# Kernel optimization log

Hardware: AMD Instinct MI355X
Metric: run time of the kernel (lower is better)

## Reference

```python
import jax, jax.numpy as jnp
import numpy as np

D_MODEL = 1024
NHEAD = 16
HEAD_DIM = D_MODEL // NHEAD


def setup_inputs() -> dict:
    key = jax.random.key(0)
    k1, k2, k3 = jax.random.split(key, 3)
    x = jax.random.normal(k1, (4, 2048, D_MODEL), dtype=jnp.float32)
    # xavier_uniform init for weights, zero bias
    lim_qkv = float(np.sqrt(6.0 / (D_MODEL + 3 * D_MODEL)))
    w_qkv = jax.random.uniform(k2, (3 * D_MODEL, D_MODEL), jnp.float32, -lim_qkv, lim_qkv)
    b_qkv = jnp.zeros((3 * D_MODEL,), jnp.float32)
    lim_o = float(np.sqrt(6.0 / (D_MODEL + D_MODEL)))
    w_o = jax.random.uniform(k3, (D_MODEL, D_MODEL), jnp.float32, -lim_o, lim_o)
    b_o = jnp.zeros((D_MODEL,), jnp.float32)
    return {"x": x, "w_qkv": w_qkv, "b_qkv": b_qkv, "w_o": w_o, "b_o": b_o}


def reference(x, w_qkv, b_qkv, w_o, b_o):
    B, S, _ = x.shape
    qkv = x @ w_qkv.T + b_qkv                      # [B,S,3D]
    qkv = qkv.reshape(B, S, NHEAD, 3 * HEAD_DIM).transpose(0, 2, 1, 3)  # [B,H,S,3d]
    q, k, v = jnp.split(qkv, 3, axis=-1)           # each [B,H,S,d]
    scale = 1.0 / jnp.sqrt(jnp.asarray(HEAD_DIM, x.dtype))
    logits = jnp.einsum('bhqd,bhkd->bhqk', q, k) * scale
    attn = jax.nn.softmax(logits, axis=-1)
    vals = jnp.einsum('bhqk,bhkd->bhqd', attn, v)  # [B,H,S,d]
    vals = vals.transpose(0, 2, 1, 3).reshape(B, S, D_MODEL)
    return vals @ w_o.T + b_o
```

## Files before the change

kernel.cpp:

```cpp
#include <hip/hip_runtime.h>
#include <hip/hip_bf16.h>
#include <stdint.h>

typedef unsigned short u16;
typedef __bf16 bf16x8 __attribute__((ext_vector_type(8)));
typedef short s16x4 __attribute__((ext_vector_type(4)));
typedef float f32x4 __attribute__((ext_vector_type(4)));
typedef u16 u16x4v __attribute__((ext_vector_type(4)));

#define AS1 __attribute__((address_space(1)))
#define AS3 __attribute__((address_space(3)))

__device__ __forceinline__ void gld_lds16(const u16* g, u16* l) {
    __builtin_amdgcn_global_load_lds((const AS1 uint32_t*)g, (AS3 uint32_t*)l, 16, 0, 0);
}

__device__ __forceinline__ u16 f2bf(float f) {
    union { float f; uint32_t u; } v; v.f = f;
    uint32_t u = v.u;
    return (u16)((u + 0x7FFFu + ((u >> 16) & 1u)) >> 16);
}

#define QSCALE 0.18033688011112042f

__global__ void cast_f32_bf16(const float* __restrict__ in, u16* __restrict__ out, int n4) {
    int i = blockIdx.x * blockDim.x + threadIdx.x;
    if (i < n4) {
        float4 f = ((const float4*)in)[i];
        u16x4v o;
        o.x = f2bf(f.x); o.y = f2bf(f.y); o.z = f2bf(f.z); o.w = f2bf(f.w);
        ((u16x4v*)out)[i] = o;
    }
}

template <int MODE>
__global__ __launch_bounds__(256, 2) void gemm_bt(
    const u16* __restrict__ A, const u16* __restrict__ B,
    const float* __restrict__ bias, float* __restrict__ Cf,
    u16* __restrict__ qb, u16* __restrict__ kb, u16* __restrict__ vT,
    int K, int ldc)
{
    __shared__ __align__(16) u16 As[128 * 32];
    __shared__ __align__(16) u16 Bs[128 * 32];
    const int tid = threadIdx.x;
    const int lane = tid & 63;
    const int w = tid >> 6;
    const int wm = (w >> 1) << 6;
    const int wn = (w & 1) << 6;
    const int r = lane & 15;
    const int q = lane >> 4;
    const int m0 = blockIdx.y << 7;
    const int n0 = blockIdx.x << 7;

    const f32x4 zero4 = {0.f, 0.f, 0.f, 0.f};
    f32x4 acc[4][4];
#pragma unroll
    for (int i = 0; i < 4; ++i)
#pragma unroll
        for (int j = 0; j < 4; ++j) acc[i][j] = zero4;

    const int nk = K >> 5;
    for (int kt = 0; kt < nk; ++kt) {
        const int kk = kt << 5;
#pragma unroll
        for (int p = 0; p < 2; ++p) {
            const int idx = (p << 8) + tid;
            const int row = idx >> 2;
            const int cg = ((idx & 3) - (row >> 1)) & 3;
            gld_lds16(A + (m0 + row) * K + kk + (cg << 3), &As[idx << 3]);
            gld_lds16(B + (n0 + row) * K + kk + (cg << 3), &Bs[idx << 3]);
        }
        __syncthreads();
        bf16x8 af[4], bf[4];
#pragma unroll
        for (int i = 0; i < 4; ++i) {
            const int ra = wm + (i << 4) + r;
            af[i] = *(const bf16x8*)&As[((ra << 2) + ((q + (ra >> 1)) & 3)) << 3];
            const int rb = wn + (i << 4) + r;
            bf[i] = *(const bf16x8*)&Bs[((rb << 2) + ((q + (rb >> 1)) & 3)) << 3];
        }
#pragma unroll
        for (int i = 0; i < 4; ++i)
#pragma unroll
            for (int j = 0; j < 4; ++j)
                acc[i][j] = __builtin_amdgcn_mfma_f32_16x16x32_bf16(af[i], bf[j], acc[i][j], 0, 0, 0);
        __syncthreads();
    }

#pragma unroll
    for (int j = 0; j < 4; ++j) {
        const int col = n0 + wn + (j << 4) + r;
        const float bv = bias[col];
        if (MODE == 0) {
#pragma unroll
            for (int i = 0; i < 4; ++i)
#pragma unroll
                for (int ii = 0; ii < 4; ++ii) {
                    const int rowg = m0 + wm + (i << 4) + (q << 2) + ii;
                    Cf[rowg * ldc + col] = acc[i][j][ii] + bv;
                }
        } else {
            const int c0 = n0 + wn + (j << 4);
            const int h = c0 / 192;
            const int rem = c0 - h * 192;
            const int region = rem >> 6;
            const int colp = (h << 6) + (rem - (region << 6)) + r;
            if (region == 0) {
#pragma unroll
                for (int i = 0; i < 4; ++i)
#pragma unroll
                    for (int ii = 0; ii < 4; ++ii) {
                        const int rowg = m0 + wm + (i << 4) + (q << 2) + ii;
                        qb[rowg * 1024 + colp] = f2bf((acc[i][j][ii] + bv) * QSCALE);
                    }
            } else if (region == 1) {
#pragma unroll
                for (int i = 0; i < 4; ++i)
#pragma unroll
                    for (int ii = 0; ii < 4; ++ii) {
                        const int rowg = m0 + wm + (i << 4) + (q << 2) + ii;
                        kb[rowg * 1024 + colp] = f2bf(acc[i][j][ii] + bv);
                    }
            } else {
#pragma unroll
                for (int i = 0; i < 4; ++i) {
                    const int rowg0 = m0 + wm + (i << 4) + (q << 2);
                    u16x4v vv;
                    vv.x = f2bf(acc[i][j][0] + bv);
                    vv.y = f2bf(acc[i][j][1] + bv);
                    vv.z = f2bf(acc[i][j][2] + bv);
                    vv.w = f2bf(acc[i][j][3] + bv);
                    *(u16x4v*)&vT[(size_t)colp * 8192 + rowg0] = vv;
                }
            }
        }
    }
}

__global__ __launch_bounds__(256, 4) void attn(
    const u16* __restrict__ qb, const u16* __restrict__ kb,
    const u16* __restrict__ vT, u16* __restrict__ vals)
{
    __shared__ __align__(16) u16 Qs[128 * 64];
    __shared__ __align__(16) u16 Ks[64 * 64];
    __shared__ __align__(16) u16 VTs[64 * 64];

    const int tid = threadIdx.x;
    const int lane = tid & 63;
    const int w = tid >> 6;
    const int r = lane & 15;
    const int q = lane >> 4;
    const int h = blockIdx.x;
    const int q0 = blockIdx.y << 7;
    const int b = blockIdx.z;
    const size_t rowbase = (size_t)b * 2048;

#pragma unroll
    for (int p = 0; p < 4; ++p) {
        const int idx = (p << 8) + tid;
        const int row = idx >> 3;
        const int cg = ((idx & 7) - row) & 7;
        gld_lds16(qb + (rowbase + q0 + row) * 1024 + (h << 6) + (cg << 3), &Qs[idx << 3]);
    }

    const f32x4 zero4 = {0.f, 0.f, 0.f, 0.f};
    f32x4 oacc[4][2];
    float lpart[2];
#pragma unroll
    for (int ht = 0; ht < 4; ++ht)
#pragma unroll
        for (int nt = 0; nt < 2; ++nt) oacc[ht][nt] = zero4;
    lpart[0] = 0.f; lpart[1] = 0.f;

    for (int kt = 0; kt < 32; ++kt) {
        const int k0 = kt << 6;
#pragma unroll
        for (int p = 0; p < 2; ++p) {
            const int idx = (p << 8) + tid;
            const int row = idx >> 3;
            const int cg = ((idx & 7) - row) & 7;
            gld_lds16(kb + (rowbase + k0 + row) * 1024 + (h << 6) + (cg << 3), &Ks[idx << 3]);
        }
#pragma unroll
        for (int p = 0; p < 2; ++p) {
            const int idx = (p << 8) + tid;
            const int hd = idx >> 3;
            const int pc = idx & 7;
            const int lc = (pc - hd - (hd >> 3)) & 7;
            gld_lds16(vT + (size_t)((h << 6) + hd) * 8192 + rowbase + k0 + (lc << 3), &VTs[idx << 3]);
        }
        __syncthreads();

        f32x4 sacc[4][2];
#pragma unroll
        for (int mt = 0; mt < 4; ++mt)
#pragma unroll
            for (int nt = 0; nt < 2; ++nt) sacc[mt][nt] = zero4;
#pragma unroll
        for (int ks = 0; ks < 2; ++ks) {
            const int L = (ks << 2) + q;
            bf16x8 bq[2], ak[4];
#pragma unroll
            for (int nt = 0; nt < 2; ++nt) {
                const int row = (w << 5) + (nt << 4) + r;
                bq[nt] = *(const bf16x8*)&Qs[(row << 6) + (((L + row) & 7) << 3)];
            }
#pragma unroll
            for (int mt = 0; mt < 4; ++mt) {
                const int row = (mt << 4) + r;
                ak[mt] = *(const bf16x8*)&Ks[(row << 6) + (((L + row) & 7) << 3)];
            }
#pragma unroll
            for (int mt = 0; mt < 4; ++mt)
#pragma unroll
                for (int nt = 0; nt < 2; ++nt)
                    sacc[mt][nt] = __builtin_amdgcn_mfma_f32_16x16x32_bf16(ak[mt], bq[nt], sacc[mt][nt], 0, 0, 0);
        }

        s16x4 pb[4][2];
#pragma unroll
        for (int mt = 0; mt < 4; ++mt) {
#pragma unroll
            for (int nt = 0; nt < 2; ++nt) {
                const float e0 = __builtin_amdgcn_exp2f(sacc[mt][nt][0]);
                const float e1 = __builtin_amdgcn_exp2f(sacc[mt][nt][1]);
                const float e2 = __builtin_amdgcn_exp2f(sacc[mt][nt][2]);
                const float e3 = __builtin_amdgcn_exp2f(sacc[mt][nt][3]);
                lpart[nt] += (e0 + e1) + (e2 + e3);
                union { __hip_bfloat162 h2[2]; s16x4 v; } u;
                u.h2[0] = __float22bfloat162_rn(float2{e0, e1});
                u.h2[1] = __float22bfloat162_rn(float2{e2, e3});
                pb[mt][nt] = u.v;
            }
        }

#pragma unroll
        for (int mt = 0; mt < 4; ++mt) {
            s16x4 av[4];
#pragma unroll
            for (int ht = 0; ht < 4; ++ht) {
                const int hd = (ht << 4) + r;
                const int chunk = (mt << 1) + (q >> 1);
                const int pc = (chunk + hd + (hd >> 3)) & 7;
                av[ht] = *(const s16x4*)&VTs[(hd << 6) + (pc << 3) + ((q & 1) << 2)];
            }
#pragma unroll
            for (int ht = 0; ht < 4; ++ht)
#pragma unroll
                for (int nt = 0; nt < 2; ++nt)
                    oacc[ht][nt] = __builtin_amdgcn_mfma_f32_16x16x16bf16_1k(av[ht], pb[mt][nt], oacc[ht][nt], 0, 0, 0);
        }
        __syncthreads();
    }

#pragma unroll
    for (int nt = 0; nt < 2; ++nt) {
        float l = lpart[nt];
        l += __shfl_xor(l, 16, 64);
        l += __shfl_xor(l, 32, 64);
        const float inv = 1.f / l;
        const int srow = q0 + (w << 5) + (nt << 4) + r;
#pragma unroll
        for (int ht = 0; ht < 4; ++ht) {
            u16x4v vv;
            vv.x = f2bf(oacc[ht][nt][0] * inv);
            vv.y = f2bf(oacc[ht][nt][1] * inv);
            vv.z = f2bf(oacc[ht][nt][2] * inv);
            vv.w = f2bf(oacc[ht][nt][3] * inv);
            const int col = (h << 6) + (ht << 4) + (q << 2);
            *(u16x4v*)&vals[(rowbase + srow) * 1024 + col] = vv;
        }
    }
}

extern "C" void kernel_launch(void* const* d_in, const int* in_sizes, int n_in,
                              void* d_out, int out_size, void* d_ws, size_t ws_size,
                              hipStream_t stream) {
    (void)in_sizes; (void)n_in; (void)out_size; (void)ws_size;
    const float* x     = (const float*)d_in[0];
    const float* w_qkv = (const float*)d_in[1];
    const float* b_qkv = (const float*)d_in[2];
    const float* w_o   = (const float*)d_in[3];
    const float* b_o   = (const float*)d_in[4];
    float* out = (float*)d_out;

    char* ws = (char*)d_ws;
    u16* xb    = (u16*)(ws);
    u16* wqkvb = (u16*)(ws + (size_t)(16 << 20));
    u16* wob   = (u16*)(ws + (size_t)(22 << 20));
    u16* qb    = (u16*)(ws + (size_t)(24 << 20));
    u16* kb    = (u16*)(ws + (size_t)(40 << 20));
    u16* vTb   = (u16*)(ws + (size_t)(56 << 20));
    u16* valsb = (u16*)(ws + (size_t)(72 << 20));

    cast_f32_bf16<<<8192, 256, 0, stream>>>(x, xb, 2097152);
    cast_f32_bf16<<<3072, 256, 0, stream>>>(w_qkv, wqkvb, 786432);
    cast_f32_bf16<<<1024, 256, 0, stream>>>(w_o, wob, 262144);

    gemm_bt<1><<<dim3(24, 64), 256, 0, stream>>>(xb, wqkvb, b_qkv, nullptr,
                                                 qb, kb, vTb, 1024, 3072);

    attn<<<dim3(16, 16, 4), 256, 0, stream>>>(qb, kb, vTb, valsb);

    gemm_bt<0><<<dim3(8, 64), 256, 0, stream>>>(valsb, wob, b_o, out,
                                                nullptr, nullptr, nullptr, 1024, 1024);
}
```

Baseline: 290.2 us.

## Double-buffer K/V tiles, hoist Q fragments, compute row sums via MFMA

The attention kernel now double-buffers the K and V^T LDS tiles, so the next tile's global-to-LDS load is issued before computing on the current one, leaving one barrier per iteration. Q fragments are loaded into registers once before the loop instead of being re-read from LDS every iteration. The softmax denominator is accumulated with an MFMA against a ones vector instead of scalar adds plus cross-lane shuffles, which also makes the sum use the bf16-rounded probabilities. LDS use grows and launch bounds drop to 3 blocks per SM, which may reduce occupancy.

```diff
diff --git a/kernel.cpp b/kernel.cpp
--- a/kernel.cpp
+++ b/kernel.cpp
@@ -137,13 +137,34 @@
     }
 }
 
-__global__ __launch_bounds__(256, 4) void attn(
+__device__ __forceinline__ void stage_kv(
+    const u16* __restrict__ kb, const u16* __restrict__ vT, u16* __restrict__ KV,
+    int tid, int h, size_t rowbase, int k0)
+{
+#pragma unroll
+    for (int p = 0; p < 2; ++p) {
+        const int idx = (p << 8) + tid;
+        const int row = idx >> 3;
+        const int cg = ((idx & 7) - row) & 7;
+        gld_lds16(kb + (rowbase + k0 + row) * 1024 + (h << 6) + (cg << 3), &KV[idx << 3]);
+    }
+#pragma unroll
+    for (int p = 0; p < 2; ++p) {
+        const int idx = (p << 8) + tid;
+        const int hd = idx >> 3;
+        const int pc = idx & 7;
+        const int lc = (pc - hd - (hd >> 3)) & 7;
+        gld_lds16(vT + (size_t)((h << 6) + hd) * 8192 + rowbase + k0 + (lc << 3),
+                  &KV[4096 + (idx << 3)]);
+    }
+}
+
+__global__ __launch_bounds__(256, 3) void attn(
     const u16* __restrict__ qb, const u16* __restrict__ kb,
     const u16* __restrict__ vT, u16* __restrict__ vals)
 {
     __shared__ __align__(16) u16 Qs[128 * 64];
-    __shared__ __align__(16) u16 Ks[64 * 64];
-    __shared__ __align__(16) u16 VTs[64 * 64];
+    __shared__ __align__(16) u16 KVs[2][2 * 4096];
 
     const int tid = threadIdx.x;
     const int lane = tid & 63;
@@ -162,34 +183,37 @@
         const int cg = ((idx & 7) - row) & 7;
         gld_lds16(qb + (rowbase + q0 + row) * 1024 + (h << 6) + (cg << 3), &Qs[idx << 3]);
     }
+    stage_kv(kb, vT, KVs[0], tid, h, rowbase, 0);
+    __syncthreads();
+
+    bf16x8 bq[2][2];
+#pragma unroll
+    for (int ks = 0; ks < 2; ++ks) {
+        const int L = (ks << 2) + q;
+#pragma unroll
+        for (int nt = 0; nt < 2; ++nt) {
+            const int row = (w << 5) + (nt << 4) + r;
+            bq[ks][nt] = *(const bf16x8*)&Qs[(row << 6) + (((L + row) & 7) << 3)];
+        }
+    }
 
     const f32x4 zero4 = {0.f, 0.f, 0.f, 0.f};
     f32x4 oacc[4][2];
-    float lpart[2];
+    f32x4 lacc[2];
 #pragma unroll
     for (int ht = 0; ht < 4; ++ht)
 #pragma unroll
         for (int nt = 0; nt < 2; ++nt) oacc[ht][nt] = zero4;
-    lpart[0] = 0.f; lpart[1] = 0.f;
+    lacc[0] = zero4; lacc[1] = zero4;
+
+    const s16x4 ones = {0x3F80, 0x3F80, 0x3F80, 0x3F80};
 
     for (int kt = 0; kt < 32; ++kt) {
-        const int k0 = kt << 6;
-#pragma unroll
-        for (int p = 0; p < 2; ++p) {
-            const int idx = (p << 8) + tid;
-            const int row = idx >> 3;
-            const int cg = ((idx & 7) - row) & 7;
-            gld_lds16(kb + (rowbase + k0 + row) * 1024 + (h << 6) + (cg << 3), &Ks[idx << 3]);
-        }
-#pragma unroll
-        for (int p = 0; p < 2; ++p) {
-            const int idx = (p << 8) + tid;
-            const int hd = idx >> 3;
-            const int pc = idx & 7;
-            const int lc = (pc - hd - (hd >> 3)) & 7;
-            gld_lds16(vT + (size_t)((h << 6) + hd) * 8192 + rowbase + k0 + (lc << 3), &VTs[idx << 3]);
-        }
-        __syncthreads();
+        const int cur = kt & 1;
+        if (kt > 0) __syncthreads();
+        if (kt < 31) stage_kv(kb, vT, KVs[cur ^ 1], tid, h, rowbase, (kt + 1) << 6);
+        const u16* Ks = KVs[cur];
+        const u16* VTs = KVs[cur] + 4096;
 
         f32x4 sacc[4][2];
 #pragma unroll
@@ -199,12 +223,7 @@
 #pragma unroll
         for (int ks = 0; ks < 2; ++ks) {
             const int L = (ks << 2) + q;
-            bf16x8 bq[2], ak[4];
-#pragma unroll
-            for (int nt = 0; nt < 2; ++nt) {
-                const int row = (w << 5) + (nt << 4) + r;
-                bq[nt] = *(const bf16x8*)&Qs[(row << 6) + (((L + row) & 7) << 3)];
-            }
+            bf16x8 ak[4];
 #pragma unroll
             for (int mt = 0; mt < 4; ++mt) {
                 const int row = (mt << 4) + r;
@@ -214,7 +233,7 @@
             for (int mt = 0; mt < 4; ++mt)
 #pragma unroll
                 for (int nt = 0; nt < 2; ++nt)
-                    sacc[mt][nt] = __builtin_amdgcn_mfma_f32_16x16x32_bf16(ak[mt], bq[nt], sacc[mt][nt], 0, 0, 0);
+                    sacc[mt][nt] = __builtin_amdgcn_mfma_f32_16x16x32_bf16(ak[mt], bq[ks][nt], sacc[mt][nt], 0, 0, 0);
         }
 
         s16x4 pb[4][2];
@@ -226,11 +245,11 @@
                 const float e1 = __builtin_amdgcn_exp2f(sacc[mt][nt][1]);
                 const float e2 = __builtin_amdgcn_exp2f(sacc[mt][nt][2]);
                 const float e3 = __builtin_amdgcn_exp2f(sacc[mt][nt][3]);
-                lpart[nt] += (e0 + e1) + (e2 + e3);
                 union { __hip_bfloat162 h2[2]; s16x4 v; } u;
                 u.h2[0] = __float22bfloat162_rn(float2{e0, e1});
                 u.h2[1] = __float22bfloat162_rn(float2{e2, e3});
                 pb[mt][nt] = u.v;
+                lacc[nt] = __builtin_amdgcn_mfma_f32_16x16x16bf16_1k(ones, pb[mt][nt], lacc[nt], 0, 0, 0);
             }
         }
 
@@ -250,15 +269,11 @@
                 for (int nt = 0; nt < 2; ++nt)
                     oacc[ht][nt] = __builtin_amdgcn_mfma_f32_16x16x16bf16_1k(av[ht], pb[mt][nt], oacc[ht][nt], 0, 0, 0);
         }
-        __syncthreads();
     }
 
 #pragma unroll
     for (int nt = 0; nt < 2; ++nt) {
-        float l = lpart[nt];
-        l += __shfl_xor(l, 16, 64);
-        l += __shfl_xor(l, 32, 64);
-        const float inv = 1.f / l;
+        const float inv = 1.f / lacc[nt][0];
         const int srow = q0 + (w << 5) + (nt << 4) + r;
 #pragma unroll
         for (int ht = 0; ht < 4; ++ht) {
```

Result: no change. 284.6 us (-2.0%).
